# Kernel optimization log

Measured on AMD Instinct MI355X. Metric: run time of the kernel, lower is better.

## Reference

```python
import jax, jax.numpy as jnp
import numpy as np

NUM_USERS = 4096
NUM_ITEMS = 8192
EMBED_DIM = 64
NUM_LAYERS = 3


def setup_inputs() -> dict:
    key = jax.random.key(0)
    k1, k2 = jax.random.split(key)
    # embedding table for users+items (nn.Embedding init normal std=0.1)
    x = jax.random.normal(k1, (NUM_USERS + NUM_ITEMS, EMBED_DIM), dtype=jnp.float32) * 0.1
    # dense 0/1 user-item interaction matrix (forward applies torch.nonzero to it)
    edge_index = jax.random.randint(k2, (NUM_USERS, NUM_ITEMS), 0, 2, dtype=jnp.int32)
    return {"x": x, "edge_index": edge_index}


def reference(x, edge_index):
    U, I, L = NUM_USERS, NUM_ITEMS, NUM_LAYERS
    adj = edge_index.astype(jnp.float32)  # [U, I], 0/1
    # symmetric degree normalization: adj / sqrt(deg_u * deg_i), nan (0/0) -> 0
    deg_u = jnp.sum(adj, axis=1)  # [U]
    deg_i = jnp.sum(adj, axis=0)  # [I]
    denom = jnp.sqrt(deg_u[:, None] * deg_i[None, :])  # [U, I]
    weights = jnp.where(denom > 0, adj / jnp.where(denom > 0, denom, 1.0), 0.0)
    # weights is identical every layer (depends only on edge_index)
    acc = jnp.zeros_like(x)
    for _ in range(L):
        # NOTE: original code concatenates (item-side, user-side) in this order
        x = jnp.concatenate([weights.T @ x[:U], weights @ x[U:]], axis=0)  # [I+U, d]
        acc = acc + x
    # alpha = 1/(1+L) * ones applied to every layer output
    return acc / (1.0 + L)
```

## Files before the change

kernel.cpp:

```cpp
#include <hip/hip_runtime.h>

#define NU 4096
#define NI 8192
#define ND 64
#define NTOT 12288
#define CT 8
#define CB 16

typedef unsigned short u16;
typedef unsigned int u32;
typedef unsigned long long u64;

__device__ __forceinline__ u16 f2bf(float f) {
    union { float f; u32 u; } v; v.f = f;
    u32 u = v.u;
    u += 0x7FFFu + ((u >> 16) & 1u);
    return (u16)(u >> 16);
}

typedef short frag8 __attribute__((ext_vector_type(8)));
typedef float f32x4 __attribute__((ext_vector_type(4)));

__global__ __launch_bounds__(256) void k_pack(const int* __restrict__ edge,
                                              u64* __restrict__ Apk) {
    __shared__ u64 wds[64][9];
    const int t = threadIdx.x, lane = t & 63, w = t >> 6;
    const int lg = lane >> 4, c4 = lane & 15;
    const int u0 = (blockIdx.x >> 4) * 64;
    const int i0 = (blockIdx.x & 15) * 512;
    const int q = (lane >> 2) & 3;

    #pragma unroll
    for (int m = 0; m < 8; m++) {
        u64 myw = 0;
        #pragma unroll
        for (int j = 0; j < 4; j++) {
            const size_t base = (size_t)(u0 + w * 16 + lg * 4 + j) * NI + i0 + m * 64 + c4;
            int v0 = edge[base];
            int v1 = edge[base + 16];
            int v2 = edge[base + 32];
            int v3 = edge[base + 48];
            u64 b0 = __ballot(v0 != 0);
            u64 b1 = __ballot(v1 != 0);
            u64 b2 = __ballot(v2 != 0);
            u64 b3 = __ballot(v3 != 0);
            u64 wd = ((b0 >> (16 * q)) & 0xFFFFULL)
                   | (((b1 >> (16 * q)) & 0xFFFFULL) << 16)
                   | (((b2 >> (16 * q)) & 0xFFFFULL) << 32)
                   | (((b3 >> (16 * q)) & 0xFFFFULL) << 48);
            if ((lane & 3) == j) myw = wd;
        }
        if (lane < 16) wds[w * 16 + lane][m] = myw;
    }
    __syncthreads();
    const int r = t >> 2, pr = t & 3;
    ulonglong2 w2;
    w2.x = wds[r][pr * 2];
    w2.y = wds[r][pr * 2 + 1];
    *(ulonglong2*)&Apk[(size_t)(u0 + r) * 128 + (i0 >> 6) + pr * 2] = w2;
}

__global__ __launch_bounds__(256) void k_bt(const u64* __restrict__ Apk,
                                            u64* __restrict__ ATpk) {
    const int t = threadIdx.x, lane = t & 63;
    const int wv = blockIdx.x * 4 + (t >> 6);
    const int g = wv >> 3;
    const int us = wv & 7;
    u64 x[8];
    #pragma unroll
    for (int tau = 0; tau < 8; tau++)
        x[tau] = Apk[(size_t)(us * 512 + tau * 64 + lane) * 128 + g];
    const u64 M[6] = {0x00000000FFFFFFFFULL, 0x0000FFFF0000FFFFULL,
                      0x00FF00FF00FF00FFULL, 0x0F0F0F0F0F0F0F0FULL,
                      0x3333333333333333ULL, 0x5555555555555555ULL};
    #pragma unroll
    for (int si = 0; si < 6; si++) {
        const int s = 32 >> si;
        #pragma unroll
        for (int tau = 0; tau < 8; tau++) {
            u64 y = __shfl_xor(x[tau], s, 64);
            x[tau] = (lane & s) ? ((x[tau] & ~M[si]) | ((y >> s) & M[si]))
                                : ((x[tau] &  M[si]) | ((y << s) & ~M[si]));
        }
    }
    #pragma unroll
    for (int qq = 0; qq < 4; qq++) {
        ulonglong2 w2; w2.x = x[2 * qq]; w2.y = x[2 * qq + 1];
        *(ulonglong2*)&ATpk[(size_t)(g * 64 + lane) * 64 + us * 8 + 2 * qq] = w2;
    }
}

__global__ __launch_bounds__(256) void k_scale0(const float* __restrict__ x,
        const u64* __restrict__ Apk, const u64* __restrict__ ATpk,
        float* __restrict__ dsu, float* __restrict__ dsi,
        u16* __restrict__ BuT, u16* __restrict__ BiT) {
    __shared__ float sc[64];
    const int t = threadIdx.x;
    const int r0 = blockIdx.x * 64;
    {
        const int rl = t >> 2, part = t & 3;
        int cnt = 0;
        if (r0 < NU) {
            const u64* p = Apk + (size_t)(r0 + rl) * 128 + part * 32;
            #pragma unroll
            for (int i = 0; i < 32; i++) cnt += (int)__popcll(p[i]);
        } else {
            const u64* p = ATpk + (size_t)(r0 - NU + rl) * 64 + part * 16;
            #pragma unroll
            for (int i = 0; i < 16; i++) cnt += (int)__popcll(p[i]);
        }
        cnt += __shfl_xor(cnt, 1, 64);
        cnt += __shfl_xor(cnt, 2, 64);
        if (part == 0) {
            float s = cnt > 0 ? rsqrtf((float)cnt) : 0.f;
            sc[rl] = s;
            if (r0 < NU) dsu[r0 + rl] = s; else dsi[r0 - NU + rl] = s;
        }
    }
    __syncthreads();
    const int r4 = t >> 4, c4 = t & 15;
    float y[4][4];
    #pragma unroll
    for (int j = 0; j < 4; j++) {
        const int rl = r4 * 4 + j;
        const float s = sc[rl];
        float4 xv = *(const float4*)(x + (size_t)(r0 + rl) * ND + c4 * 4);
        y[j][0] = xv.x * s; y[j][1] = xv.y * s;
        y[j][2] = xv.z * s; y[j][3] = xv.w * s;
    }
    u16* dst; size_t stride; int col0;
    if (r0 < NU) { dst = BuT; stride = NU; col0 = r0; }
    else         { dst = BiT; stride = NI; col0 = r0 - NU; }
    #pragma unroll
    for (int k = 0; k < 4; k++) {
        ushort4 w;
        w.x = f2bf(y[0][k]); w.y = f2bf(y[1][k]);
        w.z = f2bf(y[2][k]); w.w = f2bf(y[3][k]);
        *(ushort4*)(dst + (size_t)(c4 * 4 + k) * stride + col0 + r4 * 4) = w;
    }
}

__global__ __launch_bounds__(256) void k_gemm(
        const u64* __restrict__ Apk, const u64* __restrict__ ATpk,
        const u16* __restrict__ BuT, const u16* __restrict__ BiT,
        float* __restrict__ Ptop, float* __restrict__ Pbot) {
    __shared__ u16 Bs[64][64];
    const int t = threadIdx.x, bx = blockIdx.x;
    const int lane = t & 63, w = t >> 6, lr = lane & 15, lg = lane >> 4;
    const u64* arow; const u16* dense; int Kstr, wpr, kbase; float* Pout;
    if (bx < 1024) {
        const int tile = bx >> 3, chunk = bx & 7;
        arow = ATpk + (size_t)(tile * 64) * 64 + chunk * 8; wpr = 64;
        dense = BuT; Kstr = NU; kbase = chunk * 512;
        Pout = Ptop + ((size_t)chunk * NI + tile * 64) * ND;
    } else {
        const int b2 = bx - 1024, tile = b2 >> 4, chunk = b2 & 15;
        arow = Apk + (size_t)(tile * 64) * 128 + chunk * 8; wpr = 128;
        dense = BiT; Kstr = NI; kbase = chunk * 512;
        Pout = Pbot + ((size_t)chunk * NU + tile * 64) * ND;
    }
    const u64* myrow = arow + (size_t)(w * 16 + lr) * wpr;
    u64 aw[8];
    #pragma unroll
    for (int qq = 0; qq < 4; qq++) {
        ulonglong2 v = *(const ulonglong2*)(myrow + qq * 2);
        aw[qq * 2] = v.x; aw[qq * 2 + 1] = v.y;
    }
    f32x4 acc[4];
    #pragma unroll
    for (int i = 0; i < 4; i++) acc[i] = f32x4{0.f, 0.f, 0.f, 0.f};
    const u16* gsrc = dense + kbase;

    for (int kk = 0; kk < 8; kk++) {
        __syncthreads();
        #pragma unroll
        for (int it = 0; it < 2; it++) {
            const int idx = t + it * 256;
            const int e = idx >> 3, seg = idx & 7;
            *(uint4*)&Bs[e][((seg ^ (e & 7)) * 8)] =
                *(const uint4*)(gsrc + (size_t)e * Kstr + kk * 64 + seg * 8);
        }
        __syncthreads();
        const u32 lo = (u32)aw[kk], hi = (u32)(aw[kk] >> 32);
        const u32 byte0 = (lo >> (lg * 8)) & 0xFFu;
        const u32 byte1 = (hi >> (lg * 8)) & 0xFFu;
        frag8 bf0, bf1;
        #pragma unroll
        for (int j = 0; j < 8; j++) {
            bf0[j] = (short)(((byte0 >> j) & 1u) ? 0x3F80 : 0);
            bf1[j] = (short)(((byte1 >> j) & 1u) ? 0x3F80 : 0);
        }
        #pragma unroll
        for (int nt = 0; nt < 4; nt++) {
            const int e = nt * 16 + lr, sw = e & 7;
            frag8 a0 = *(const frag8*)&Bs[e][(lg ^ sw) * 8];
            frag8 a1 = *(const frag8*)&Bs[e][((4 + lg) ^ sw) * 8];
            acc[nt] = __builtin_amdgcn_mfma_f32_16x16x32_bf16(a0, bf0, acc[nt], 0, 0, 0);
            acc[nt] = __builtin_amdgcn_mfma_f32_16x16x32_bf16(a1, bf1, acc[nt], 0, 0, 0);
        }
    }
    #pragma unroll
    for (int nt = 0; nt < 4; nt++)
        *(f32x4*)&Pout[(size_t)(w * 16 + lr) * ND + nt * 16 + lg * 4] = acc[nt];
}

__global__ __launch_bounds__(256) void k_reduce(
        const float* __restrict__ Ptop, const float* __restrict__ Pbot,
        const float* __restrict__ dsu, const float* __restrict__ dsi,
        float* __restrict__ accbuf, u16* __restrict__ BuTn,
        u16* __restrict__ BiTn, float* __restrict__ out, int layer) {
    __shared__ u16 TB[64][24];
    const int t = threadIdx.x, bx = blockIdx.x;
    const int rl = t >> 4, e4 = t & 15;
    int grow; float so;
    float sx = 0.f, sy = 0.f, sz = 0.f, sw = 0.f;
    if (bx < 512) {
        grow = bx * 16 + rl;
        const float* p = Ptop + (size_t)grow * ND + e4 * 4;
        #pragma unroll
        for (int c = 0; c < CT; c++) {
            float4 v = *(const float4*)(p + (size_t)c * NI * ND);
            sx += v.x; sy += v.y; sz += v.z; sw += v.w;
        }
        so = dsi[grow];
    } else {
        const int u = (bx - 512) * 16 + rl;
        grow = NI + u;
        const float* p = Pbot + (size_t)u * ND + e4 * 4;
        #pragma unroll
        for (int c = 0; c < CB; c++) {
            float4 v = *(const float4*)(p + (size_t)c * NU * ND);
            sx += v.x; sy += v.y; sz += v.z; sw += v.w;
        }
        so = dsu[grow - NI];
    }
    float4 y;
    y.x = sx * so; y.y = sy * so; y.z = sz * so; y.w = sw * so;
    const size_t o = (size_t)grow * ND + e4 * 4;
    if (layer == 0) {
        *(float4*)(accbuf + o) = y;
    } else if (layer == 1) {
        float4 a = *(const float4*)(accbuf + o);
        a.x += y.x; a.y += y.y; a.z += y.z; a.w += y.w;
        *(float4*)(accbuf + o) = a;
    } else {
        float4 a = *(const float4*)(accbuf + o);
        a.x = (a.x + y.x) * 0.25f; a.y = (a.y + y.y) * 0.25f;
        a.z = (a.z + y.z) * 0.25f; a.w = (a.w + y.w) * 0.25f;
        *(float4*)(out + o) = a;
    }
    if (layer != 2) {
        const float fn = (grow < NU) ? dsu[grow] : dsi[grow - NU];
        TB[e4 * 4 + 0][rl] = f2bf(y.x * fn);
        TB[e4 * 4 + 1][rl] = f2bf(y.y * fn);
        TB[e4 * 4 + 2][rl] = f2bf(y.z * fn);
        TB[e4 * 4 + 3][rl] = f2bf(y.w * fn);
        __syncthreads();
        if (t < 128) {
            const int e = t >> 1, h = t & 1;
            u16* dst; size_t stride; int col0;
            if (bx < 256)      { dst = BuTn; stride = NU; col0 = bx * 16; }
            else if (bx < 512) { dst = BiTn; stride = NI; col0 = bx * 16 - NU; }
            else               { dst = BiTn; stride = NI; col0 = (bx - 512) * 16 + NI - NU; }
            uint4 v = *(const uint4*)&TB[e][h * 8];
            *(uint4*)(dst + (size_t)e * stride + col0 + h * 8) = v;
        }
    }
}

extern "C" void kernel_launch(void* const* d_in, const int* in_sizes, int n_in,
                              void* d_out, int out_size, void* d_ws, size_t ws_size,
                              hipStream_t stream) {
    (void)in_sizes; (void)n_in; (void)out_size; (void)ws_size;
    const float* x    = (const float*)d_in[0];
    const int*   edge = (const int*)d_in[1];
    float* out = (float*)d_out;

    char* ws = (char*)d_ws;
    size_t off = 0;
    u64* Apk  = (u64*)(ws + off); off += (size_t)NU * (NI / 64) * 8;
    u64* ATpk = (u64*)(ws + off); off += (size_t)NI * (NU / 64) * 8;
    float* dsu = (float*)(ws + off); off += (size_t)NU * 4;
    float* dsi = (float*)(ws + off); off += (size_t)NI * 4;
    u16* BuT0 = (u16*)(ws + off); off += (size_t)ND * NU * 2;
    u16* BuT1 = (u16*)(ws + off); off += (size_t)ND * NU * 2;
    u16* BiT0 = (u16*)(ws + off); off += (size_t)ND * NI * 2;
    u16* BiT1 = (u16*)(ws + off); off += (size_t)ND * NI * 2;
    float* acc  = (float*)(ws + off); off += (size_t)NTOT * ND * 4;
    float* Ptop = (float*)(ws + off); off += (size_t)CT * NI * ND * 4;
    float* Pbot = (float*)(ws + off); off += (size_t)CB * NU * ND * 4;

    k_pack<<<1024, 256, 0, stream>>>(edge, Apk);
    k_bt<<<256, 256, 0, stream>>>(Apk, ATpk);
    k_scale0<<<NTOT / 64, 256, 0, stream>>>(x, Apk, ATpk, dsu, dsi, BuT0, BiT0);

    k_gemm<<<2048, 256, 0, stream>>>(Apk, ATpk, BuT0, BiT0, Ptop, Pbot);
    k_reduce<<<768, 256, 0, stream>>>(Ptop, Pbot, dsu, dsi, acc, BuT1, BiT1, out, 0);
    k_gemm<<<2048, 256, 0, stream>>>(Apk, ATpk, BuT1, BiT1, Ptop, Pbot);
    k_reduce<<<768, 256, 0, stream>>>(Ptop, Pbot, dsu, dsi, acc, BuT0, BiT0, out, 1);
    k_gemm<<<2048, 256, 0, stream>>>(Apk, ATpk, BuT0, BiT0, Ptop, Pbot);
    k_reduce<<<768, 256, 0, stream>>>(Ptop, Pbot, dsu, dsi, acc,
                                      (u16*)nullptr, (u16*)nullptr, out, 2);
}
```

Before: 298.8 us.

## Fuse bit-packing with transpose and preload full dense tile in GEMM

Merges the pack and bit-transpose kernels into one kernel. It reads int4 vectors of the edge matrix, packs bits into shared memory, and writes both the row-packed and transposed bitmaps without re-reading Apk from global memory. The GEMM now loads the whole 64x512 bf16 dense slab into 64KB of LDS once, replacing the per-k-step sync-and-load loop. That removes 16 barriers per block, but the larger LDS footprint lowers occupancy and stops loads from overlapping with MFMA work.

```diff
diff --git a/kernel.cpp b/kernel.cpp
--- a/kernel.cpp
+++ b/kernel.cpp
@@ -21,72 +21,69 @@
 typedef short frag8 __attribute__((ext_vector_type(8)));
 typedef float f32x4 __attribute__((ext_vector_type(4)));
 
-__global__ __launch_bounds__(256) void k_pack(const int* __restrict__ edge,
-                                              u64* __restrict__ Apk) {
-    __shared__ u64 wds[64][9];
-    const int t = threadIdx.x, lane = t & 63, w = t >> 6;
-    const int lg = lane >> 4, c4 = lane & 15;
-    const int u0 = (blockIdx.x >> 4) * 64;
+__global__ __launch_bounds__(256) void k_pack2(const int* __restrict__ edge,
+        u64* __restrict__ Apk, u64* __restrict__ ATpk) {
+    __shared__ __align__(16) u16 At[256][40];
+    __shared__ __align__(16) u64 Tt[512][6];
+    const int t = threadIdx.x;
+    const int u0 = (blockIdx.x >> 4) * 256;
     const int i0 = (blockIdx.x & 15) * 512;
-    const int q = (lane >> 2) & 3;
-
-    #pragma unroll
-    for (int m = 0; m < 8; m++) {
-        u64 myw = 0;
-        #pragma unroll
-        for (int j = 0; j < 4; j++) {
-            const size_t base = (size_t)(u0 + w * 16 + lg * 4 + j) * NI + i0 + m * 64 + c4;
-            int v0 = edge[base];
-            int v1 = edge[base + 16];
-            int v2 = edge[base + 32];
-            int v3 = edge[base + 48];
-            u64 b0 = __ballot(v0 != 0);
-            u64 b1 = __ballot(v1 != 0);
-            u64 b2 = __ballot(v2 != 0);
-            u64 b3 = __ballot(v3 != 0);
-            u64 wd = ((b0 >> (16 * q)) & 0xFFFFULL)
-                   | (((b1 >> (16 * q)) & 0xFFFFULL) << 16)
-                   | (((b2 >> (16 * q)) & 0xFFFFULL) << 32)
-                   | (((b3 >> (16 * q)) & 0xFFFFULL) << 48);
-            if ((lane & 3) == j) myw = wd;
-        }
-        if (lane < 16) wds[w * 16 + lane][m] = myw;
+    const int cg = t & 31;
+    const int rb = t >> 5;
+
+    #pragma unroll 4
+    for (int rr = 0; rr < 32; rr++) {
+        const int row = rb * 32 + rr;
+        const int4* p = (const int4*)(edge + (size_t)(u0 + row) * NI + i0 + cg * 16);
+        u32 bits = 0;
+        #pragma unroll
+        for (int m = 0; m < 4; m++) {
+            int4 v = p[m];
+            bits |= (v.x != 0 ? 1u : 0u) << (m * 4 + 0);
+            bits |= (v.y != 0 ? 1u : 0u) << (m * 4 + 1);
+            bits |= (v.z != 0 ? 1u : 0u) << (m * 4 + 2);
+            bits |= (v.w != 0 ? 1u : 0u) << (m * 4 + 3);
+        }
+        At[row][cg] = (u16)bits;
     }
     __syncthreads();
-    const int r = t >> 2, pr = t & 3;
-    ulonglong2 w2;
-    w2.x = wds[r][pr * 2];
-    w2.y = wds[r][pr * 2 + 1];
-    *(ulonglong2*)&Apk[(size_t)(u0 + r) * 128 + (i0 >> 6) + pr * 2] = w2;
-}
-
-__global__ __launch_bounds__(256) void k_bt(const u64* __restrict__ Apk,
-                                            u64* __restrict__ ATpk) {
-    const int t = threadIdx.x, lane = t & 63;
-    const int wv = blockIdx.x * 4 + (t >> 6);
-    const int g = wv >> 3;
-    const int us = wv & 7;
-    u64 x[8];
-    #pragma unroll
-    for (int tau = 0; tau < 8; tau++)
-        x[tau] = Apk[(size_t)(us * 512 + tau * 64 + lane) * 128 + g];
-    const u64 M[6] = {0x00000000FFFFFFFFULL, 0x0000FFFF0000FFFFULL,
-                      0x00FF00FF00FF00FFULL, 0x0F0F0F0F0F0F0F0FULL,
-                      0x3333333333333333ULL, 0x5555555555555555ULL};
-    #pragma unroll
-    for (int si = 0; si < 6; si++) {
-        const int s = 32 >> si;
-        #pragma unroll
-        for (int tau = 0; tau < 8; tau++) {
-            u64 y = __shfl_xor(x[tau], s, 64);
-            x[tau] = (lane & s) ? ((x[tau] & ~M[si]) | ((y >> s) & M[si]))
-                                : ((x[tau] &  M[si]) | ((y << s) & ~M[si]));
-        }
-    }
-    #pragma unroll
-    for (int qq = 0; qq < 4; qq++) {
-        ulonglong2 w2; w2.x = x[2 * qq]; w2.y = x[2 * qq + 1];
-        *(ulonglong2*)&ATpk[(size_t)(g * 64 + lane) * 64 + us * 8 + 2 * qq] = w2;
+
+    {
+        u64* dst = Apk + (size_t)(u0 + t) * 128 + (i0 >> 6);
+        #pragma unroll
+        for (int q = 0; q < 4; q++) {
+            uint4 v = *(const uint4*)&At[t][q * 8];
+            *(uint4*)(dst + q * 2) = v;
+        }
+    }
+
+    {
+        const int lane = t & 63, w = t >> 6;
+        const u64 M[6] = {0x00000000FFFFFFFFULL, 0x0000FFFF0000FFFFULL,
+                          0x00FF00FF00FF00FFULL, 0x0F0F0F0F0F0F0F0FULL,
+                          0x3333333333333333ULL, 0x5555555555555555ULL};
+        #pragma unroll
+        for (int sc = 0; sc < 8; sc++) {
+            u64 x = *(const u64*)&At[w * 64 + lane][sc * 4];
+            #pragma unroll
+            for (int si = 0; si < 6; si++) {
+                const int s = 32 >> si;
+                u64 y = __shfl_xor(x, s, 64);
+                x = (lane & s) ? ((x & ~M[si]) | ((y >> s) & M[si]))
+                               : ((x &  M[si]) | ((y << s) & ~M[si]));
+            }
+            Tt[sc * 64 + lane][w] = x;
+        }
+    }
+    __syncthreads();
+    #pragma unroll
+    for (int j = 0; j < 2; j++) {
+        const int item = t * 2 + j;
+        ulonglong2 a = *(const ulonglong2*)&Tt[item][0];
+        ulonglong2 b = *(const ulonglong2*)&Tt[item][2];
+        u64* dst = ATpk + (size_t)(i0 + item) * 64 + (u0 >> 6);
+        *(ulonglong2*)dst = a;
+        *(ulonglong2*)(dst + 2) = b;
     }
 }
 
@@ -144,7 +141,7 @@
         const u64* __restrict__ Apk, const u64* __restrict__ ATpk,
         const u16* __restrict__ BuT, const u16* __restrict__ BiT,
         float* __restrict__ Ptop, float* __restrict__ Pbot) {
-    __shared__ u16 Bs[64][64];
+    __shared__ __align__(16) u16 Bs[64][512];
     const int t = threadIdx.x, bx = blockIdx.x;
     const int lane = t & 63, w = t >> 6, lr = lane & 15, lg = lane >> 4;
     const u64* arow; const u16* dense; int Kstr, wpr, kbase; float* Pout;
@@ -166,21 +163,22 @@
         ulonglong2 v = *(const ulonglong2*)(myrow + qq * 2);
         aw[qq * 2] = v.x; aw[qq * 2 + 1] = v.y;
     }
+    const u16* gsrc = dense + kbase;
+    #pragma unroll
+    for (int it = 0; it < 16; it++) {
+        const int idx = t + it * 256;
+        const int e = idx >> 6, seg = idx & 63;
+        const int kk = seg >> 3, s8 = seg & 7;
+        *(uint4*)&Bs[e][kk * 64 + ((s8 ^ (e & 7)) * 8)] =
+            *(const uint4*)(gsrc + (size_t)e * Kstr + seg * 8);
+    }
     f32x4 acc[4];
     #pragma unroll
     for (int i = 0; i < 4; i++) acc[i] = f32x4{0.f, 0.f, 0.f, 0.f};
-    const u16* gsrc = dense + kbase;
-
+    __syncthreads();
+
+    #pragma unroll
     for (int kk = 0; kk < 8; kk++) {
-        __syncthreads();
-        #pragma unroll
-        for (int it = 0; it < 2; it++) {
-            const int idx = t + it * 256;
-            const int e = idx >> 3, seg = idx & 7;
-            *(uint4*)&Bs[e][((seg ^ (e & 7)) * 8)] =
-                *(const uint4*)(gsrc + (size_t)e * Kstr + kk * 64 + seg * 8);
-        }
-        __syncthreads();
         const u32 lo = (u32)aw[kk], hi = (u32)(aw[kk] >> 32);
         const u32 byte0 = (lo >> (lg * 8)) & 0xFFu;
         const u32 byte1 = (hi >> (lg * 8)) & 0xFFu;
@@ -193,8 +191,8 @@
         #pragma unroll
         for (int nt = 0; nt < 4; nt++) {
             const int e = nt * 16 + lr, sw = e & 7;
-            frag8 a0 = *(const frag8*)&Bs[e][(lg ^ sw) * 8];
-            frag8 a1 = *(const frag8*)&Bs[e][((4 + lg) ^ sw) * 8];
+            frag8 a0 = *(const frag8*)&Bs[e][kk * 64 + ((lg ^ sw) * 8)];
+            frag8 a1 = *(const frag8*)&Bs[e][kk * 64 + (((4 + lg) ^ sw) * 8)];
             acc[nt] = __builtin_amdgcn_mfma_f32_16x16x32_bf16(a0, bf0, acc[nt], 0, 0, 0);
             acc[nt] = __builtin_amdgcn_mfma_f32_16x16x32_bf16(a1, bf1, acc[nt], 0, 0, 0);
         }
@@ -290,8 +288,7 @@
     float* Ptop = (float*)(ws + off); off += (size_t)CT * NI * ND * 4;
     float* Pbot = (float*)(ws + off); off += (size_t)CB * NU * ND * 4;
 
-    k_pack<<<1024, 256, 0, stream>>>(edge, Apk);
-    k_bt<<<256, 256, 0, stream>>>(Apk, ATpk);
+    k_pack2<<<256, 256, 0, stream>>>(edge, Apk, ATpk);
     k_scale0<<<NTOT / 64, 256, 0, stream>>>(x, Apk, ATpk, dsu, dsi, BuT0, BiT0);
 
     k_gemm<<<2048, 256, 0, stream>>>(Apk, ATpk, BuT0, BiT0, Ptop, Pbot);
```

Measured after the change: 293.7 us. No clear change (-1.7%).
